# Kernel optimization log

Hardware: AMD Instinct MI355X
Metric: run time of the kernel (lower is better)

The kernel has to match this reference:

```python
import jax, jax.numpy as jnp
import numpy as np

NUM_HEADS = 8
CHUNK = 64


def _retention(q, k, v):
    # q, k: (B, H, L, DK); v: (B, H, L, DV). Chunked linear retention with
    # per-head exponential decay gamma_h = 1 - 2^(-5-h) (RetNet convention).
    B, Hn, L, DK = q.shape
    DV = v.shape[-1]
    C = CHUNK
    N = L // C
    dt = q.dtype
    gamma = (1.0 - jnp.exp2(-5.0 - jnp.arange(Hn, dtype=jnp.float32))).astype(dt)  # (H,)
    q = q * (DK ** -0.5)
    idx = jnp.arange(C)
    diff = idx[:, None] - idx[None, :]
    # intra-chunk causal decay mask D[h,i,j] = gamma_h^(i-j) for i>=j else 0
    D = jnp.where(diff >= 0, gamma[:, None, None] ** diff, 0.0).astype(dt)      # (H,C,C)
    decay_q = (gamma[:, None] ** (idx[None, :] + 1)).astype(dt)                 # (H,C)
    decay_k = (gamma[:, None] ** (C - 1 - idx[None, :])).astype(dt)             # (H,C)
    decay_s = (gamma ** C).astype(dt)                                           # (H,)

    def to_chunks(x):
        return jnp.moveaxis(x.reshape(B, Hn, N, C, -1), 2, 0)  # (N,B,H,C,d)

    qs, ks, vs = map(to_chunks, (q, k, v))

    def step(S, x):
        qc, kc, vc = x  # (B,H,C,dk) / (B,H,C,dv)
        attn = jnp.einsum('bhid,bhjd->bhij', qc, kc) * D
        o_intra = jnp.einsum('bhij,bhje->bhie', attn, vc)
        o_inter = jnp.einsum('bhid,bhde->bhie', qc * decay_q[None, :, :, None], S)
        S_new = decay_s[None, :, None, None] * S + jnp.einsum(
            'bhjd,bhje->bhde', kc * decay_k[None, :, :, None], vc)
        return S_new, o_intra + o_inter

    S0 = jnp.zeros((B, Hn, DK, DV), dt)
    _, o = jax.lax.scan(step, S0, (qs, ks, vs))  # (N,B,H,C,DV)
    return jnp.moveaxis(o, 0, 2).reshape(B, Hn, L, DV)


def _xavier(key, fan_in, fan_out, gain=2 ** (-2.5)):
    limit = gain * np.sqrt(6.0 / (fan_in + fan_out))
    return jax.random.uniform(key, (fan_in, fan_out), jnp.float32, -limit, limit)


def setup_inputs() -> dict:
    key = jax.random.key(0)
    k0, k1, k2, k3, k4 = jax.random.split(key, 5)
    B, L, D = 2, 4096, 1024
    return {
        'hidden_states': jax.random.normal(k0, (B, L, D), jnp.float32),
        'rel_pos': jnp.zeros((1,), jnp.float32),  # unused by the module's forward
        'Wq': _xavier(k1, D, D),
        'Wk': _xavier(k2, D, D),
        'Wv': _xavier(k3, D, D),
        'Wo': _xavier(k4, D, D),
    }


def reference(hidden_states, rel_pos, Wq, Wk, Wv, Wo):
    B, L, Dm = hidden_states.shape
    Hd = Dm // NUM_HEADS
    q = (hidden_states @ Wq).reshape(B, L, NUM_HEADS, Hd).transpose(0, 2, 1, 3)
    k = (hidden_states @ Wk).reshape(B, L, NUM_HEADS, Hd).transpose(0, 2, 1, 3)
    v = (hidden_states @ Wv).reshape(B, L, NUM_HEADS, Hd).transpose(0, 2, 1, 3)
    o = _retention(q, k, v)  # (B,H,L,Hd)
    o = o.transpose(0, 2, 1, 3).reshape(B, L, Dm)
    return o @ Wo
```

## Files before the change

### kernel.cpp

```cpp
#include <hip/hip_runtime.h>
#include <hip/hip_bf16.h>

typedef __bf16 bf16;
typedef __bf16 bf16x8 __attribute__((ext_vector_type(8)));
typedef float f32x4 __attribute__((ext_vector_type(4)));

#define MFMA16(a, b, c) __builtin_amdgcn_mfma_f32_16x16x32_bf16((a), (b), (c), 0, 0, 0)


__device__ __forceinline__ void g2l16(const bf16* g, bf16* l) {
  __builtin_amdgcn_global_load_lds(
      (const __attribute__((address_space(1))) void*)g,
      (__attribute__((address_space(3))) void*)l, 16, 0, 0);
}

__device__ __forceinline__ int swz72(int row, int c) {
  return row * 72 + (c & 7) + ((((c >> 3) ^ (row >> 3)) & 7) << 3);
}

__global__ __launch_bounds__(256) void prep(
    const float* __restrict__ X, const float* __restrict__ Wq,
    const float* __restrict__ Wk, const float* __restrict__ Wv,
    const float* __restrict__ Wo, bf16* __restrict__ Xb,
    bf16* __restrict__ Wt) {
  __shared__ bf16 t[64 * 72];
  const int tid = threadIdx.x;
  if (blockIdx.x < 4096) {
    const size_t i = ((size_t)blockIdx.x * 256 + tid) * 8;
    float4 a = *(const float4*)&X[i];
    float4 b = *(const float4*)&X[i + 4];
    union { bf16 h[8]; uint4 u; } p;
    p.h[0] = (bf16)a.x; p.h[1] = (bf16)a.y; p.h[2] = (bf16)a.z; p.h[3] = (bf16)a.w;
    p.h[4] = (bf16)b.x; p.h[5] = (bf16)b.y; p.h[6] = (bf16)b.z; p.h[7] = (bf16)b.w;
    *(uint4*)&Xb[i] = p.u;
    return;
  }
  const int bid2 = blockIdx.x - 4096;
  const int bx = bid2 & 15, by = (bid2 >> 4) & 15, bz = bid2 >> 8;
  const float* src = (bz == 0) ? Wq : (bz == 1) ? Wk : (bz == 2) ? Wv : Wo;
  bf16* dst = Wt + (size_t)bz * 1024 * 1024;
  const int k0 = bx * 64, n0 = by * 64;
#pragma unroll
  for (int s = 0; s < 4; ++s) {
    int u = tid + s * 256;
    int r = u >> 4, c4 = (u & 15) * 4;
    float4 f = *(const float4*)&src[(size_t)(k0 + r) * 1024 + n0 + c4];
    t[r * 72 + c4 + 0] = (bf16)f.x;
    t[r * 72 + c4 + 1] = (bf16)f.y;
    t[r * 72 + c4 + 2] = (bf16)f.z;
    t[r * 72 + c4 + 3] = (bf16)f.w;
  }
  __syncthreads();
#pragma unroll
  for (int s = 0; s < 2; ++s) {
    int u = tid + s * 256;
    int r = u >> 3, cc = u & 7;
    union { bf16 h[8]; uint4 u4; } pk;
#pragma unroll
    for (int j = 0; j < 8; ++j) pk.h[j] = t[(cc * 8 + j) * 72 + r];
    *(uint4*)&dst[(size_t)(n0 + r) * 1024 + k0 + cc * 8] = pk.u4;
  }
}

template <typename TC, int QKV>
__global__ __launch_bounds__(256) void gemm_lds(
    const bf16* __restrict__ A, const bf16* __restrict__ Bt,
    TC* __restrict__ C, float alpha) {
  __shared__ bf16 lA[128 * 64];
  __shared__ bf16 lB[128 * 64];
  const int m0 = blockIdx.x * 128, n0 = blockIdx.y * 128;
  if (QKV) {
    Bt += (size_t)blockIdx.z * 1024 * 1024;
    C += (size_t)blockIdx.z * 8192 * 1024;
    if (blockIdx.z != 0) alpha = 1.0f;
  }
  const int tid = threadIdx.x;
  const int w = tid >> 6, lane = tid & 63, lr = lane & 15, quad = lane >> 4;
  const int wm = w >> 1, wn = w & 1;

  const int srow = w * 32 + (lane >> 3);
  const int clog = (lane & 7) ^ ((lane >> 3) & 7);
  const bf16* gA = A + (size_t)(m0 + srow) * 1024 + clog * 8;
  const bf16* gB = Bt + (size_t)(n0 + srow) * 1024 + clog * 8;

  f32x4 acc[4][4] = {};

  for (int it = 0; it < 16; ++it) {
    const int k0 = it * 64;
#pragma unroll
    for (int is = 0; is < 4; ++is) {
      g2l16(gA + (size_t)is * 8 * 1024 + k0, &lA[(w * 32 + is * 8) * 64]);
      g2l16(gB + (size_t)is * 8 * 1024 + k0, &lB[(w * 32 + is * 8) * 64]);
    }
    __syncthreads();
#pragma unroll
    for (int kk = 0; kk < 2; ++kk) {
      bf16x8 af[4], bfv[4];
#pragma unroll
      for (int i = 0; i < 4; ++i) {
        const int m = wm * 64 + i * 16 + lr;
        af[i] = *(bf16x8*)&lA[m * 64 + (((kk * 4 + quad) ^ (lr & 7)) * 8)];
      }
#pragma unroll
      for (int j = 0; j < 4; ++j) {
        const int n = wn * 64 + j * 16 + lr;
        bfv[j] = *(bf16x8*)&lB[n * 64 + (((kk * 4 + quad) ^ (lr & 7)) * 8)];
      }
#pragma unroll
      for (int i = 0; i < 4; ++i)
#pragma unroll
        for (int j = 0; j < 4; ++j)
          acc[i][j] = MFMA16(af[i], bfv[j], acc[i][j]);
    }
    __syncthreads();
  }
#pragma unroll
  for (int i = 0; i < 4; ++i) {
#pragma unroll
    for (int j = 0; j < 4; ++j) {
      const int row = m0 + wm * 64 + i * 16 + quad * 4;
      const int col = n0 + wn * 64 + j * 16 + lr;
#pragma unroll
      for (int r = 0; r < 4; ++r)
        C[(size_t)(row + r) * 1024 + col] = (TC)(acc[i][j][r] * alpha);
    }
  }
}

__global__ __launch_bounds__(256) void chunk_kv(
    const bf16* __restrict__ kb, const bf16* __restrict__ vb,
    bf16* __restrict__ Tb) {
  __shared__ bf16 lK[128 * 72];
  __shared__ bf16 lV[128 * 72];
  const int g = blockIdx.x;
  const int bh = g >> 6, n = g & 63, b = bh >> 3, h = bh & 7;
  const float log2g = log2f(1.0f - exp2f(-5.0f - (float)h));
  const int tid = threadIdx.x;
  const size_t rowbase = (size_t)(b * 4096 + n * 64) * 1024 + h * 128;
  const bf16* kc = kb + rowbase;
  const bf16* vc = vb + rowbase;
#pragma unroll
  for (int s = 0; s < 4; ++s) {
    int u = tid + s * 256;
    int c = u >> 4, d0 = (u & 15) * 8;
    union { uint4 u4; bf16 h8[8]; } kv, vv;
    kv.u4 = *(const uint4*)&kc[(size_t)c * 1024 + d0];
    vv.u4 = *(const uint4*)&vc[(size_t)c * 1024 + d0];
    const float dec = exp2f((float)(63 - c) * log2g);
#pragma unroll
    for (int j = 0; j < 8; ++j) {
      lK[swz72(d0 + j, c)] = (bf16)((float)kv.h8[j] * dec);
      lV[swz72(d0 + j, c)] = vv.h8[j];
    }
  }
  __syncthreads();
  const int w = tid >> 6, lane = tid & 63, lr = lane & 15, quad = lane >> 4;
  const int wm = w >> 1, wn = w & 1;
  f32x4 acc[4][4] = {};
#pragma unroll
  for (int kk = 0; kk < 2; ++kk) {
    bf16x8 af[4], bv[4];
#pragma unroll
    for (int i = 0; i < 4; ++i)
      af[i] = *(bf16x8*)&lK[swz72(wm * 64 + i * 16 + lr, kk * 32 + quad * 8)];
#pragma unroll
    for (int j = 0; j < 4; ++j)
      bv[j] = *(bf16x8*)&lV[swz72(wn * 64 + j * 16 + lr, kk * 32 + quad * 8)];
#pragma unroll
    for (int i = 0; i < 4; ++i)
#pragma unroll
      for (int j = 0; j < 4; ++j)
        acc[i][j] = MFMA16(af[i], bv[j], acc[i][j]);
  }
  bf16* tchunk = Tb + (size_t)g * 16384;
#pragma unroll
  for (int i = 0; i < 4; ++i) {
#pragma unroll
    for (int j = 0; j < 4; ++j) {
      const int dk = wm * 64 + i * 16 + quad * 4;
      const int dv = wn * 64 + j * 16 + lr;
      union { bf16 h4[4]; uint2 u2; } pk;
#pragma unroll
      for (int r = 0; r < 4; ++r) pk.h4[r] = (bf16)acc[i][j][r];
      *(uint2*)&tchunk[(size_t)dv * 128 + dk] = pk.u2;
    }
  }
}

__global__ __launch_bounds__(256) void scan_state(bf16* __restrict__ Tb) {
  const int blk = blockIdx.x;
  const int bh = blk >> 3, seg = blk & 7, h = bh & 7;
  const float gs = exp2f(64.0f * log2f(1.0f - exp2f(-5.0f - (float)h)));
  const size_t base = (size_t)bh * 64 * 16384 + (size_t)seg * 2048 +
                      (size_t)threadIdx.x * 8;
  float S[8] = {0.f, 0.f, 0.f, 0.f, 0.f, 0.f, 0.f, 0.f};
#pragma unroll 4
  for (int n = 0; n < 64; ++n) {
    const size_t a = base + (size_t)n * 16384;
    union { uint4 u4; bf16 h8[8]; } in, out;
    in.u4 = *(const uint4*)&Tb[a];
#pragma unroll
    for (int e = 0; e < 8; ++e) {
      out.h8[e] = (bf16)S[e];
      S[e] = gs * S[e] + (float)in.h8[e];
    }
    *(uint4*)&Tb[a] = out.u4;
  }
}

__global__ __launch_bounds__(256) void chunk_out(
    const bf16* __restrict__ qb, const bf16* __restrict__ kb,
    const bf16* __restrict__ vb, const bf16* __restrict__ Sp,
    bf16* __restrict__ ob) {
  __shared__ bf16 lQ[64 * 136];
  __shared__ bf16 lQd[64 * 136];
  __shared__ bf16 lK[64 * 136];
  __shared__ bf16 lVt[128 * 72];
  __shared__ bf16 lP[64 * 72];
  const int g = blockIdx.x;
  const int bh = g >> 6, n = g & 63, b = bh >> 3, h = bh & 7;
  const float log2g = log2f(1.0f - exp2f(-5.0f - (float)h));
  const int tid = threadIdx.x;
  const size_t rowbase = (size_t)(b * 4096 + n * 64) * 1024 + h * 128;
  const bf16* qc = qb + rowbase;
  const bf16* kc = kb + rowbase;
  const bf16* vc = vb + rowbase;
#pragma unroll
  for (int s = 0; s < 4; ++s) {
    int u = tid + s * 256;
    int c = u >> 4, d0 = (u & 15) * 8;
    union { uint4 u4; bf16 h8[8]; } qv, vv, qd;
    qv.u4 = *(const uint4*)&qc[(size_t)c * 1024 + d0];
    *(uint4*)&lQ[c * 136 + d0] = qv.u4;
    *(uint4*)&lK[c * 136 + d0] = *(const uint4*)&kc[(size_t)c * 1024 + d0];
    const float dq = exp2f((float)(c + 1) * log2g);
#pragma unroll
    for (int j = 0; j < 8; ++j) qd.h8[j] = (bf16)((float)qv.h8[j] * dq);
    *(uint4*)&lQd[c * 136 + d0] = qd.u4;
    vv.u4 = *(const uint4*)&vc[(size_t)c * 1024 + d0];
#pragma unroll
    for (int j = 0; j < 8; ++j) lVt[swz72(d0 + j, c)] = vv.h8[j];
  }
  __syncthreads();
  const int w = tid >> 6, lane = tid & 63, lr = lane & 15, quad = lane >> 4;

  f32x4 p[4] = {};
#pragma unroll
  for (int kk = 0; kk < 4; ++kk) {
    bf16x8 bfrag = *(bf16x8*)&lK[(w * 16 + lr) * 136 + kk * 32 + quad * 8];
#pragma unroll
    for (int i = 0; i < 4; ++i) {
      bf16x8 afrag = *(bf16x8*)&lQ[(i * 16 + lr) * 136 + kk * 32 + quad * 8];
      p[i] = MFMA16(afrag, bfrag, p[i]);
    }
  }
#pragma unroll
  for (int i = 0; i < 4; ++i) {
#pragma unroll
    for (int r = 0; r < 4; ++r) {
      const int row = i * 16 + quad * 4 + r;
      const int col = w * 16 + lr;
      const int diff = row - col;
      const float val =
          (diff >= 0) ? p[i][r] * exp2f((float)diff * log2g) : 0.0f;
      lP[row * 72 + col] = (bf16)val;
    }
  }
  __syncthreads();

  f32x4 oacc[4][2] = {};
#pragma unroll
  for (int j = 0; j < 2; ++j) {
    const int dvt = w * 32 + j * 16;
#pragma unroll
    for (int kk = 0; kk < 2; ++kk) {
      bf16x8 bfrag = *(bf16x8*)&lVt[swz72(dvt + lr, kk * 32 + quad * 8)];
#pragma unroll
      for (int i = 0; i < 4; ++i) {
        bf16x8 afrag = *(bf16x8*)&lP[(i * 16 + lr) * 72 + kk * 32 + quad * 8];
        oacc[i][j] = MFMA16(afrag, bfrag, oacc[i][j]);
      }
    }
  }

  const bf16* sp = Sp + (size_t)g * 16384;
#pragma unroll
  for (int kk = 0; kk < 4; ++kk) {
    bf16x8 aN[4];
#pragma unroll
    for (int i = 0; i < 4; ++i)
      aN[i] = *(bf16x8*)&lQd[(i * 16 + lr) * 136 + kk * 32 + quad * 8];
#pragma unroll
    for (int j = 0; j < 2; ++j) {
      bf16x8 bfrag =
          *(const bf16x8*)&sp[(size_t)(w * 32 + j * 16 + lr) * 128 + kk * 32 + quad * 8];
#pragma unroll
      for (int i = 0; i < 4; ++i) oacc[i][j] = MFMA16(aN[i], bfrag, oacc[i][j]);
    }
  }

  bf16* oc = ob + rowbase;
#pragma unroll
  for (int i = 0; i < 4; ++i)
#pragma unroll
    for (int j = 0; j < 2; ++j)
#pragma unroll
      for (int r = 0; r < 4; ++r) {
        const int row = i * 16 + quad * 4 + r;
        const int col = w * 32 + j * 16 + lr;
        oc[(size_t)row * 1024 + col] = (bf16)oacc[i][j][r];
      }
}

extern "C" void kernel_launch(void* const* d_in, const int* in_sizes, int n_in,
                              void* d_out, int out_size, void* d_ws,
                              size_t ws_size, hipStream_t stream) {
  const float* X  = (const float*)d_in[0];
  const float* Wq = (const float*)d_in[2];
  const float* Wk = (const float*)d_in[3];
  const float* Wv = (const float*)d_in[4];
  const float* Wo = (const float*)d_in[5];

  char* ws = (char*)d_ws;
  const size_t SZ_QKV = (size_t)8192 * 1024 * sizeof(bf16);
  bf16* qb = (bf16*)(ws);
  bf16* ob = (bf16*)(ws + 3 * SZ_QKV);
  bf16* Tb = (bf16*)(ws + 4 * SZ_QKV);
  bf16* Wt = (bf16*)(ws + 6 * SZ_QKV);
  bf16* Xb = (bf16*)(ws + 6 * SZ_QKV + (size_t)4 * 1024 * 1024 * sizeof(bf16));
  bf16* kb = qb + (size_t)8192 * 1024;
  bf16* vb = kb + (size_t)8192 * 1024;

  prep<<<5120, 256, 0, stream>>>(X, Wq, Wk, Wv, Wo, Xb, Wt);

  const float qscale = 0.08838834764831845f;
  gemm_lds<bf16, 1><<<dim3(64, 8, 3), 256, 0, stream>>>(Xb, Wt, qb, qscale);

  chunk_kv<<<1024, 256, 0, stream>>>(kb, vb, Tb);
  scan_state<<<128, 256, 0, stream>>>(Tb);
  chunk_out<<<1024, 256, 0, stream>>>(qb, kb, vb, Tb, ob);

  gemm_lds<float, 0><<<dim3(64, 8), 256, 0, stream>>>(
      ob, Wt + (size_t)3 * 1024 * 1024, (float*)d_out, 1.0f);
}
```

Measured before the change: 229.7 us.

## Replace QKV GEMM with 256x256-tile 8-wave ping-pong pipelined kernel

```diff
diff --git a/kernel.cpp b/kernel.cpp
--- a/kernel.cpp
+++ b/kernel.cpp
@@ -59,6 +59,126 @@
 #pragma unroll
     for (int j = 0; j < 8; ++j) pk.h[j] = t[(cc * 8 + j) * 72 + r];
     *(uint4*)&dst[(size_t)(n0 + r) * 1024 + k0 + cc * 8] = pk.u4;
+  }
+}
+
+template <typename TC, int QKV>
+__global__ __launch_bounds__(512, 2) void gemm_8p(
+    const bf16* __restrict__ A, const bf16* __restrict__ Bt,
+    TC* __restrict__ C, float alpha) {
+  __shared__ bf16 lds[2 * 32768];
+  const int m0 = blockIdx.x * 256;
+  const int n0g = blockIdx.y * 256;
+  int ncol0 = n0g;
+  if (QKV) {
+    const int z = n0g >> 10;
+    C += (size_t)z * (8192 * 1024);
+    if (z != 0) alpha = 1.0f;
+    ncol0 = n0g & 1023;
+  }
+  const int tid = threadIdx.x;
+  const int w = tid >> 6, lane = tid & 63, lr = lane & 15, quad = lane >> 4;
+  const int wm = w >> 2, wn = w & 3;
+  const int l8 = lane >> 3;
+  const int clog = (lane & 7) ^ l8;
+  const bf16* gA = A + (size_t)(m0 + l8) * 1024 + clog * 8;
+  const bf16* gB = Bt + (size_t)(n0g + l8) * 1024 + clog * 8;
+
+#define SA(tt, bi, mh) do {                                                  \
+    { const int r_ = (mh)*64 + (w & 7)*8;                                    \
+      g2l16(gA + (size_t)r_*1024 + (tt)*64, &lds[(bi)*32768 + r_*64]); }     \
+    { const int r_ = (mh)*64 + (w & 7)*8 + 128;                              \
+      g2l16(gA + (size_t)r_*1024 + (tt)*64, &lds[(bi)*32768 + r_*64]); }     \
+  } while (0)
+#define SB(tt, bi, nh) do {                                                  \
+    { const int bb = w;                                                      \
+      const int r_ = (bb>>2)*64 + (nh)*32 + (bb&3)*8;                        \
+      g2l16(gB + (size_t)r_*1024 + (tt)*64,                                  \
+            &lds[(bi)*32768 + 16384 + r_*64]); }                             \
+    { const int bb = w + 8;                                                  \
+      const int r_ = (bb>>2)*64 + (nh)*32 + (bb&3)*8;                        \
+      g2l16(gB + (size_t)r_*1024 + (tt)*64,                                  \
+            &lds[(bi)*32768 + 16384 + r_*64]); }                             \
+  } while (0)
+#define LA_(dst, bi, mh)                                                     \
+  _Pragma("unroll") for (int i = 0; i < 4; ++i)                              \
+  _Pragma("unroll") for (int kk = 0; kk < 2; ++kk)                           \
+    dst[i][kk] = *(const bf16x8*)&lds[(bi)*32768 +                           \
+        (wm*128 + (mh)*64 + i*16 + lr)*64 + (((kk*4+quad)^(lr&7))*8)];
+#define LB_(dst, bi, nh)                                                     \
+  _Pragma("unroll") for (int j = 0; j < 2; ++j)                              \
+  _Pragma("unroll") for (int kk = 0; kk < 2; ++kk)                           \
+    dst[j][kk] = *(const bf16x8*)&lds[(bi)*32768 + 16384 +                   \
+        (wn*64 + (nh)*32 + j*16 + lr)*64 + (((kk*4+quad)^(lr&7))*8)];
+#define MM_(mh, nh, Af, Bf)                                                  \
+  __builtin_amdgcn_s_setprio(1);                                             \
+  _Pragma("unroll") for (int i = 0; i < 4; ++i)                              \
+  _Pragma("unroll") for (int j = 0; j < 2; ++j)                              \
+  _Pragma("unroll") for (int kk = 0; kk < 2; ++kk)                           \
+    acc[(mh)*4+i][(nh)*2+j] =                                                \
+        MFMA16(Af[i][kk], Bf[j][kk], acc[(mh)*4+i][(nh)*2+j]);               \
+  __builtin_amdgcn_s_setprio(0);
+#define BAR   asm volatile("s_barrier" ::: "memory")
+#define LGKM0 asm volatile("s_waitcnt lgkmcnt(0)" ::: "memory")
+#define VM6   asm volatile("s_waitcnt vmcnt(6)" ::: "memory")
+#define VM0   asm volatile("s_waitcnt vmcnt(0)" ::: "memory")
+
+  f32x4 acc[8][4] = {};
+  bf16x8 a_[4][2], b0_[2][2], b1_[2][2];
+
+  SA(0, 0, 0); SB(0, 0, 0); SA(0, 0, 1); SB(0, 0, 1);
+  SA(1, 1, 0); SB(1, 1, 0); SB(1, 1, 1);
+  VM6; BAR;
+
+#pragma unroll 1
+  for (int t = 0; t < 8; ++t) {
+    LA_(a_, 0, 0); LB_(b0_, 0, 0);
+    SA(2 * t + 1, 1, 1);
+    BAR; LGKM0; MM_(0, 0, a_, b0_); BAR;
+    LB_(b1_, 0, 1);
+    if (t < 7) SA(2 * t + 2, 0, 0);
+    BAR; LGKM0; MM_(0, 1, a_, b1_); BAR;
+    LA_(a_, 0, 1);
+    if (t < 7) SB(2 * t + 2, 0, 0);
+    BAR; LGKM0; MM_(1, 0, a_, b0_); BAR;
+    if (t < 7) SA(2 * t + 2, 0, 1);
+    BAR; LGKM0; MM_(1, 1, a_, b1_);
+    if (t < 7) { VM6; } else { VM0; }
+    BAR;
+    LA_(a_, 1, 0); LB_(b0_, 1, 0);
+    if (t < 7) SB(2 * t + 2, 0, 1);
+    BAR; LGKM0; MM_(0, 0, a_, b0_); BAR;
+    LB_(b1_, 1, 1);
+    if (t < 7) SA(2 * t + 3, 1, 0);
+    BAR; LGKM0; MM_(0, 1, a_, b1_); BAR;
+    LA_(a_, 1, 1);
+    if (t < 7) SB(2 * t + 3, 1, 0);
+    BAR; LGKM0; MM_(1, 0, a_, b0_); BAR;
+    if (t < 7) SB(2 * t + 3, 1, 1);
+    BAR; LGKM0; MM_(1, 1, a_, b1_);
+    VM6;
+    BAR;
+  }
+#undef SA
+#undef SB
+#undef LA_
+#undef LB_
+#undef MM_
+#undef BAR
+#undef LGKM0
+#undef VM6
+#undef VM0
+
+#pragma unroll
+  for (int a = 0; a < 8; ++a) {
+#pragma unroll
+    for (int b = 0; b < 4; ++b) {
+      const int row = m0 + wm * 128 + (a >> 2) * 64 + (a & 3) * 16 + quad * 4;
+      const int col = ncol0 + wn * 64 + (b >> 1) * 32 + (b & 1) * 16 + lr;
+#pragma unroll
+      for (int r = 0; r < 4; ++r)
+        C[(size_t)(row + r) * 1024 + col] = (TC)(acc[a][b][r] * alpha);
+    }
   }
 }
 
@@ -334,7 +454,7 @@
   prep<<<5120, 256, 0, stream>>>(X, Wq, Wk, Wv, Wo, Xb, Wt);
 
   const float qscale = 0.08838834764831845f;
-  gemm_lds<bf16, 1><<<dim3(64, 8, 3), 256, 0, stream>>>(Xb, Wt, qb, qscale);
+  gemm_8p<bf16, 1><<<dim3(32, 12), 512, 0, stream>>>(Xb, Wt, qb, qscale);
 
   chunk_kv<<<1024, 256, 0, stream>>>(kb, vb, Tb);
   scan_state<<<128, 256, 0, stream>>>(Tb);
```

Measured after the change: 236.3 us. 2.9% more time.

## Fuse chunk KV outer products with sequential state scan into one kernel

Applied to the files above, without the earlier changes.

```diff
diff --git a/kernel.cpp b/kernel.cpp
--- a/kernel.cpp
+++ b/kernel.cpp
@@ -127,84 +127,75 @@
   }
 }
 
-__global__ __launch_bounds__(256) void chunk_kv(
+__global__ __launch_bounds__(512) void chunk_kv_scan(
     const bf16* __restrict__ kb, const bf16* __restrict__ vb,
     bf16* __restrict__ Tb) {
-  __shared__ bf16 lK[128 * 72];
-  __shared__ bf16 lV[128 * 72];
-  const int g = blockIdx.x;
-  const int bh = g >> 6, n = g & 63, b = bh >> 3, h = bh & 7;
+  __shared__ bf16 lK[2][128 * 72];
+  __shared__ bf16 lV[2][64 * 72];
+  const int bh = blockIdx.x >> 1, half = blockIdx.x & 1;
+  const int b = bh >> 3, h = bh & 7, dv0 = half * 64;
   const float log2g = log2f(1.0f - exp2f(-5.0f - (float)h));
+  const float gs = exp2f(64.0f * log2g);
   const int tid = threadIdx.x;
-  const size_t rowbase = (size_t)(b * 4096 + n * 64) * 1024 + h * 128;
-  const bf16* kc = kb + rowbase;
-  const bf16* vc = vb + rowbase;
-#pragma unroll
-  for (int s = 0; s < 4; ++s) {
-    int u = tid + s * 256;
-    int c = u >> 4, d0 = (u & 15) * 8;
-    union { uint4 u4; bf16 h8[8]; } kv, vv;
-    kv.u4 = *(const uint4*)&kc[(size_t)c * 1024 + d0];
-    vv.u4 = *(const uint4*)&vc[(size_t)c * 1024 + d0];
-    const float dec = exp2f((float)(63 - c) * log2g);
+
+  const int kc0 = tid >> 4;
+  const int kd0 = (tid & 15) * 8;
+  const int kc1 = kc0 + 32;
+  const float dec0 = exp2f((float)(63 - kc0) * log2g);
+  const float dec1 = exp2f((float)(63 - kc1) * log2g);
+  const int vc0 = tid >> 3;
+  const int ve0 = (tid & 7) * 8;
+
+  const bf16* kp = kb + (size_t)(b * 4096) * 1024 + h * 128;
+  const bf16* vp = vb + (size_t)(b * 4096) * 1024 + h * 128 + dv0;
+  bf16* tp = Tb + (size_t)(bh * 64) * 16384;
+
+  const int w = tid >> 6, lane = tid & 63, lr = lane & 15, quad = lane >> 4;
+  const int wr = w >> 2, wc = w & 3;
+
+  f32x4 Sreg[4] = {};
+  uint4 kr0 = *(const uint4*)&kp[(size_t)kc0 * 1024 + kd0];
+  uint4 kr1 = *(const uint4*)&kp[(size_t)kc1 * 1024 + kd0];
+  uint4 vr  = *(const uint4*)&vp[(size_t)vc0 * 1024 + ve0];
+
+  for (int n = 0; n < 64; ++n) {
+    const int bi = n & 1;
+    union { uint4 u4; bf16 h8[8]; } t0, t1, tv;
+    t0.u4 = kr0; t1.u4 = kr1; tv.u4 = vr;
 #pragma unroll
     for (int j = 0; j < 8; ++j) {
-      lK[swz72(d0 + j, c)] = (bf16)((float)kv.h8[j] * dec);
-      lV[swz72(d0 + j, c)] = vv.h8[j];
-    }
-  }
-  __syncthreads();
-  const int w = tid >> 6, lane = tid & 63, lr = lane & 15, quad = lane >> 4;
-  const int wm = w >> 1, wn = w & 1;
-  f32x4 acc[4][4] = {};
-#pragma unroll
-  for (int kk = 0; kk < 2; ++kk) {
-    bf16x8 af[4], bv[4];
-#pragma unroll
-    for (int i = 0; i < 4; ++i)
-      af[i] = *(bf16x8*)&lK[swz72(wm * 64 + i * 16 + lr, kk * 32 + quad * 8)];
-#pragma unroll
-    for (int j = 0; j < 4; ++j)
-      bv[j] = *(bf16x8*)&lV[swz72(wn * 64 + j * 16 + lr, kk * 32 + quad * 8)];
-#pragma unroll
-    for (int i = 0; i < 4; ++i)
-#pragma unroll
-      for (int j = 0; j < 4; ++j)
-        acc[i][j] = MFMA16(af[i], bv[j], acc[i][j]);
-  }
-  bf16* tchunk = Tb + (size_t)g * 16384;
-#pragma unroll
-  for (int i = 0; i < 4; ++i) {
-#pragma unroll
-    for (int j = 0; j < 4; ++j) {
-      const int dk = wm * 64 + i * 16 + quad * 4;
-      const int dv = wn * 64 + j * 16 + lr;
+      lK[bi][swz72(kd0 + j, kc0)] = (bf16)((float)t0.h8[j] * dec0);
+      lK[bi][swz72(kd0 + j, kc1)] = (bf16)((float)t1.h8[j] * dec1);
+      lV[bi][swz72(ve0 + j, vc0)] = tv.h8[j];
+    }
+    __syncthreads();
+    if (n < 63) {
+      const size_t roff = (size_t)(n + 1) * 64 * 1024;
+      kr0 = *(const uint4*)&kp[roff + (size_t)kc0 * 1024 + kd0];
+      kr1 = *(const uint4*)&kp[roff + (size_t)kc1 * 1024 + kd0];
+      vr  = *(const uint4*)&vp[roff + (size_t)vc0 * 1024 + ve0];
+    }
+    f32x4 acc[4] = {};
+#pragma unroll
+    for (int kk = 0; kk < 2; ++kk) {
+      bf16x8 bv = *(bf16x8*)&lV[bi][swz72(wc * 16 + lr, kk * 32 + quad * 8)];
+#pragma unroll
+      for (int i = 0; i < 4; ++i) {
+        bf16x8 af =
+            *(bf16x8*)&lK[bi][swz72(wr * 64 + i * 16 + lr, kk * 32 + quad * 8)];
+        acc[i] = MFMA16(af, bv, acc[i]);
+      }
+    }
+    bf16* tc = tp + (size_t)n * 16384;
+#pragma unroll
+    for (int i = 0; i < 4; ++i) {
       union { bf16 h4[4]; uint2 u2; } pk;
 #pragma unroll
-      for (int r = 0; r < 4; ++r) pk.h4[r] = (bf16)acc[i][j][r];
-      *(uint2*)&tchunk[(size_t)dv * 128 + dk] = pk.u2;
-    }
-  }
-}
-
-__global__ __launch_bounds__(256) void scan_state(bf16* __restrict__ Tb) {
-  const int blk = blockIdx.x;
-  const int bh = blk >> 3, seg = blk & 7, h = bh & 7;
-  const float gs = exp2f(64.0f * log2f(1.0f - exp2f(-5.0f - (float)h)));
-  const size_t base = (size_t)bh * 64 * 16384 + (size_t)seg * 2048 +
-                      (size_t)threadIdx.x * 8;
-  float S[8] = {0.f, 0.f, 0.f, 0.f, 0.f, 0.f, 0.f, 0.f};
-#pragma unroll 4
-  for (int n = 0; n < 64; ++n) {
-    const size_t a = base + (size_t)n * 16384;
-    union { uint4 u4; bf16 h8[8]; } in, out;
-    in.u4 = *(const uint4*)&Tb[a];
-#pragma unroll
-    for (int e = 0; e < 8; ++e) {
-      out.h8[e] = (bf16)S[e];
-      S[e] = gs * S[e] + (float)in.h8[e];
-    }
-    *(uint4*)&Tb[a] = out.u4;
+      for (int r = 0; r < 4; ++r) pk.h4[r] = (bf16)Sreg[i][r];
+      *(uint2*)&tc[(size_t)(dv0 + wc * 16 + lr) * 128 + wr * 64 + i * 16 +
+                   quad * 4] = pk.u2;
+      Sreg[i] = gs * Sreg[i] + acc[i];
+    }
   }
 }
 
@@ -336,8 +327,8 @@
   const float qscale = 0.08838834764831845f;
   gemm_lds<bf16, 1><<<dim3(64, 8, 3), 256, 0, stream>>>(Xb, Wt, qb, qscale);
 
-  chunk_kv<<<1024, 256, 0, stream>>>(kb, vb, Tb);
-  scan_state<<<128, 256, 0, stream>>>(Tb);
+  chunk_kv_scan<<<32, 512, 0, stream>>>(kb, vb, Tb);
+
   chunk_out<<<1024, 256, 0, stream>>>(qb, kb, vb, Tb, ob);
 
   gemm_lds<float, 0><<<dim3(64, 8), 256, 0, stream>>>(
```

Result: slower. 306.1 us (+33.3%).
